# Optimization experiments

Hardware: AMD Instinct MI355X
Metric: run time of the kernel (lower is better)

Reference implementation:

```python
import jax, jax.numpy as jnp
import numpy as np

N_NODES = 50000
N_EDGES = 800000
D = 128
BN_EPS = 1e-5


def gcn_conv(x, src, dst, W, b, n_nodes):
    # x: [N, Din]; src/dst: [E+N] (self-loops already appended)
    h = x @ W  # [N, Dout]
    deg = jax.ops.segment_sum(jnp.ones_like(src, dtype=h.dtype), dst, num_segments=n_nodes)
    dinv = jnp.where(deg > 0, jax.lax.rsqrt(deg), 0.0)  # deg^{-1/2}
    norm = dinv[src] * dinv[dst]  # [E+N]
    msg = h[src] * norm[:, None]  # gather + scale
    out = jax.ops.segment_sum(msg, dst, num_segments=n_nodes)  # scatter-add
    return out + b


def batchnorm_prelu(x, gamma, beta, a):
    # training-mode BN over node dim (biased variance), then PReLU
    mu = jnp.mean(x, axis=0)
    var = jnp.mean(jnp.square(x - mu), axis=0)
    xn = (x - mu) * jax.lax.rsqrt(var + BN_EPS)
    y = xn * gamma + beta
    return jnp.where(y >= 0, y, a * y)


def setup_inputs():
    key = jax.random.key(0)
    ks = jax.random.split(key, 8)
    x = jax.random.normal(ks[0], (N_NODES, D), dtype=jnp.float32)
    edge_index = jax.random.randint(ks[1], (2, N_EDGES), 0, N_NODES, dtype=jnp.int32)
    lim = float(np.sqrt(6.0 / (D + D)))  # glorot
    W1 = jax.random.uniform(ks[2], (D, D), jnp.float32, -lim, lim)
    W2 = jax.random.uniform(ks[3], (D, D), jnp.float32, -lim, lim)
    b1 = jnp.zeros((D,), jnp.float32)
    b2 = jnp.zeros((D,), jnp.float32)
    gamma1 = jnp.ones((D,), jnp.float32)
    beta1 = jnp.zeros((D,), jnp.float32)
    gamma2 = jnp.ones((D,), jnp.float32)
    beta2 = jnp.zeros((D,), jnp.float32)
    a1 = jnp.full((1,), 0.25, jnp.float32)
    a2 = jnp.full((1,), 0.25, jnp.float32)
    return {"x": x, "edge_index": edge_index, "W1": W1, "b1": b1, "gamma1": gamma1,
            "beta1": beta1, "a1": a1, "W2": W2, "b2": b2, "gamma2": gamma2,
            "beta2": beta2, "a2": a2}


def reference(x, edge_index, W1, b1, gamma1, beta1, a1, W2, b2, gamma2, beta2, a2):
    n = x.shape[0]
    loops = jnp.arange(n, dtype=edge_index.dtype)
    src = jnp.concatenate([edge_index[0], loops])
    dst = jnp.concatenate([edge_index[1], loops])
    h = gcn_conv(x, src, dst, W1, b1, n)
    h = batchnorm_prelu(h, gamma1, beta1, a1)
    h = gcn_conv(h, src, dst, W2, b2, n)
    h = batchnorm_prelu(h, gamma2, beta2, a2)
    return h
```

## Files before the change

### kernel.cpp

```cpp
#include <hip/hip_runtime.h>
#include <hip/hip_bf16.h>

#define N_NODES 50000
#define N_EDGES 800000
#define D 128
#define BN_EPS 1e-5f
#define GEMM_ROWS 128
#define LDS_PITCH 136

#define BSH 8
#define NB 196
#define TILE 4096
#define NTILES ((N_EDGES + TILE - 1) / TILE)
#define REC_CAP 6144

typedef unsigned short u16;
typedef short bf16x8 __attribute__((ext_vector_type(8)));
typedef float f32x4  __attribute__((ext_vector_type(4)));

__device__ __forceinline__ u16 f2bf(float f) {
    union { float f; unsigned int u; } v; v.f = f;
    unsigned int u = v.u;
    return (u16)((u + 0x7FFF + ((u >> 16) & 1)) >> 16);
}
__device__ __forceinline__ float bflo(unsigned int u) {
    union { unsigned int u; float f; } v; v.u = u << 16; return v.f;
}
__device__ __forceinline__ float bfhi(unsigned int u) {
    union { unsigned int u; float f; } v; v.u = u & 0xFFFF0000u; return v.f;
}
__device__ __forceinline__ unsigned int packbf(float a, float b) {
    return (unsigned int)f2bf(a) | ((unsigned int)f2bf(b) << 16);
}

__global__ __launch_bounds__(256) void hist_prep(const int* __restrict__ dst,
                                                 const float* __restrict__ W1,
                                                 const float* __restrict__ W2,
                                                 int* __restrict__ thist,
                                                 u16* __restrict__ Wt1,
                                                 u16* __restrict__ Wt2,
                                                 float* __restrict__ sums) {
    __shared__ int h[256];
    const int t = threadIdx.x;
    const int b = blockIdx.x;
    if (b < NTILES) {
        h[t] = 0;
        __syncthreads();
        const int e0 = b * TILE;
#pragma unroll
        for (int i = 0; i < 16; ++i) {
            int e = e0 + t + 256 * i;
            if (e < N_EDGES) atomicAdd(&h[dst[e] >> BSH], 1);
        }
        __syncthreads();
        thist[b * 256 + t] = h[t];
    } else {
        const int wb = b - NTILES;
        if (wb == 0) { sums[t] = 0.f; sums[256 + t] = 0.f; }
        int u = wb * 256 + t;
        const float* W = (u < 16384) ? W1 : W2;
        u16* Wt        = (u < 16384) ? Wt1 : Wt2;
        int v = u & 16383;
        int k = v >> 7, n = v & 127;
        Wt[n * 128 + k] = f2bf(W[v]);
    }
}

__global__ __launch_bounds__(256) void bucket_scan(const int* __restrict__ thist,
                                                   int* __restrict__ btot,
                                                   int* __restrict__ bbase,
                                                   int* __restrict__ bcur,
                                                   int* __restrict__ row_ptr) {
    __shared__ int s[256];
    const int t = threadIdx.x;
    int v = 0;
    for (int i = 0; i < NTILES; ++i) v += thist[i * 256 + t];
    s[t] = v;
    __syncthreads();
#pragma unroll
    for (int off = 1; off < 256; off <<= 1) {
        int add = (t >= off) ? s[t - off] : 0;
        __syncthreads();
        s[t] += add;
        __syncthreads();
    }
    if (t < NB) { btot[t] = v; bbase[t] = s[t] - v; bcur[t] = s[t] - v; }
    if (t == 0) row_ptr[N_NODES] = N_EDGES;
}

__global__ __launch_bounds__(256) void bucket_scatter(const int* __restrict__ src,
                                                      const int* __restrict__ dst,
                                                      int* __restrict__ bcur,
                                                      unsigned int* __restrict__ brec) {
    __shared__ int h[256];
    __shared__ int sb[256];
    __shared__ int lbase[256];
    __shared__ int lcur[256];
    __shared__ int gbase[256];
    __shared__ unsigned int  rec[TILE];
    __shared__ unsigned char rbk[TILE];
    const int t  = threadIdx.x;
    const int e0 = blockIdx.x * TILE;
    const int tcount = min(TILE, N_EDGES - e0);

    h[t] = 0;
    __syncthreads();

    unsigned int myrec[16];
    int          myb[16];
#pragma unroll
    for (int i = 0; i < 16; ++i) {
        int e = e0 + t + 256 * i;
        if (e < N_EDGES) {
            unsigned int s_ = (unsigned int)src[e];
            unsigned int d_ = (unsigned int)dst[e];
            int b = (int)(d_ >> BSH);
            myb[i]   = b;
            myrec[i] = s_ | ((d_ & 255u) << 16);
            atomicAdd(&h[b], 1);
        } else myb[i] = -1;
    }
    __syncthreads();
    sb[t] = h[t];
    __syncthreads();
#pragma unroll
    for (int off = 1; off < 256; off <<= 1) {
        int add = (t >= off) ? sb[t - off] : 0;
        __syncthreads();
        sb[t] += add;
        __syncthreads();
    }
    lbase[t] = sb[t] - h[t];
    lcur[t]  = sb[t] - h[t];
    __syncthreads();
#pragma unroll
    for (int i = 0; i < 16; ++i) {
        if (myb[i] >= 0) {
            int p = atomicAdd(&lcur[myb[i]], 1);
            rec[p] = myrec[i];
            rbk[p] = (unsigned char)myb[i];
        }
    }
    __syncthreads();
    if (t < NB && h[t] > 0) gbase[t] = atomicAdd(&bcur[t], h[t]);
    __syncthreads();
    for (int i = t; i < tcount; i += 256) {
        int b = rbk[i];
        brec[gbase[b] + (i - lbase[b])] = rec[i];
    }
}

__global__ __launch_bounds__(256) void bucket_csr(const unsigned int* __restrict__ brec,
                                                  const int* __restrict__ bbase,
                                                  const int* __restrict__ btot,
                                                  int* __restrict__ row_ptr,
                                                  u16* __restrict__ col,
                                                  float* __restrict__ dinv) {
    __shared__ unsigned int rec[REC_CAP];
    __shared__ u16 cls[REC_CAP];
    __shared__ int h[256];
    __shared__ int sb[256];
    __shared__ int lcur[256];
    const int b    = blockIdx.x;
    const int t    = threadIdx.x;
    const int base = bbase[b];
    const int cnt  = min(btot[b], REC_CAP);
    const int n0   = b << BSH;
    const int nn   = min(256, N_NODES - n0);

    for (int i = t; i < cnt; i += 256) rec[i] = brec[base + i];
    h[t] = 0;
    __syncthreads();
    for (int i = t; i < cnt; i += 256) atomicAdd(&h[(rec[i] >> 16) & 255u], 1);
    __syncthreads();
    sb[t] = h[t];
    __syncthreads();
#pragma unroll
    for (int off = 1; off < 256; off <<= 1) {
        int add = (t >= off) ? sb[t - off] : 0;
        __syncthreads();
        sb[t] += add;
        __syncthreads();
    }
    int excl = sb[t] - h[t];
    lcur[t] = excl;
    if (t < nn) {
        row_ptr[n0 + t] = base + excl;
        dinv[n0 + t]    = rsqrtf((float)h[t] + 1.0f);
    }
    __syncthreads();
    for (int i = t; i < cnt; i += 256) {
        unsigned int r = rec[i];
        int p = atomicAdd(&lcur[(r >> 16) & 255u], 1);
        cls[p] = (u16)(r & 0xFFFFu);
    }
    __syncthreads();
    for (int i = t; i < cnt; i += 256) col[base + i] = cls[i];
}

template <bool BN_IN>
__global__ __launch_bounds__(256) void gemm_bf16(const void* __restrict__ Xv,
                                                 const u16* __restrict__ Wt,
                                                 u16* __restrict__ C,
                                                 const float* __restrict__ dinv,
                                                 const float* __restrict__ sums,
                                                 const float* __restrict__ gamma,
                                                 const float* __restrict__ beta,
                                                 const float* __restrict__ a,
                                                 int nrows) {
    __shared__ u16 As[GEMM_ROWS * LDS_PITCH];
    __shared__ u16 Ws[128 * LDS_PITCH];
    const int tid  = threadIdx.x;
    const int row0 = blockIdx.x * GEMM_ROWS;
    const float invN = 1.0f / (float)N_NODES;

    const bf16x8* Wt8 = (const bf16x8*)Wt;
#pragma unroll
    for (int i = 0; i < 8; ++i) {
        int u = tid + 256 * i;
        int n = u >> 4, kg = u & 15;
        *(bf16x8*)&Ws[n * LDS_PITCH + kg * 8] = Wt8[u];
    }

    if (BN_IN) {
        const uint4* X4 = (const uint4*)Xv;
        const float av = a[0];
#pragma unroll
        for (int i = 0; i < 8; ++i) {
            int u    = tid + 256 * i;
            int r    = u >> 4, kg = u & 15;
            int grow = row0 + r;
            uint4 o = make_uint4(0, 0, 0, 0);
            if (grow < nrows) {
                uint4 v = X4[(size_t)grow * 16 + kg];
                float f[8] = { bflo(v.x), bfhi(v.x), bflo(v.y), bfhi(v.y),
                               bflo(v.z), bfhi(v.z), bflo(v.w), bfhi(v.w) };
#pragma unroll
                for (int c = 0; c < 8; ++c) {
                    int fe     = kg * 8 + c;
                    float mean = sums[fe] * invN;
                    float var  = sums[128 + fe] * invN - mean * mean;
                    float sc   = rsqrtf(var + BN_EPS) * gamma[fe];
                    float y    = (f[c] - mean) * sc + beta[fe];
                    f[c]       = (y >= 0.f) ? y : av * y;
                }
                o.x = packbf(f[0], f[1]); o.y = packbf(f[2], f[3]);
                o.z = packbf(f[4], f[5]); o.w = packbf(f[6], f[7]);
            }
            *(uint4*)&As[r * LDS_PITCH + kg * 8] = o;
        }
    } else {
        const float4* X4 = (const float4*)Xv;
#pragma unroll
        for (int i = 0; i < 16; ++i) {
            int u    = tid + 256 * i;
            int r    = u >> 5, kf = u & 31;
            int grow = row0 + r;
            float4 v = make_float4(0.f, 0.f, 0.f, 0.f);
            if (grow < nrows) v = X4[(size_t)grow * 32 + kf];
            ushort4 p;
            p.x = f2bf(v.x); p.y = f2bf(v.y); p.z = f2bf(v.z); p.w = f2bf(v.w);
            *(ushort4*)&As[r * LDS_PITCH + kf * 4] = p;
        }
    }
    __syncthreads();

    const int wv   = tid >> 6;
    const int lane = tid & 63;
    const int n    = lane & 15;
    const int q    = lane >> 4;
    const int c0   = wv * 32;

    bf16x8 bfr[4][2];
#pragma unroll
    for (int kb = 0; kb < 4; ++kb)
#pragma unroll
        for (int c = 0; c < 2; ++c)
            bfr[kb][c] = *(const bf16x8*)&Ws[(c0 + 16 * c + n) * LDS_PITCH + 32 * kb + 8 * q];

    f32x4 acc[8][2];
    const f32x4 z = {0.f, 0.f, 0.f, 0.f};
#pragma unroll
    for (int rt = 0; rt < 8; ++rt) { acc[rt][0] = z; acc[rt][1] = z; }

#pragma unroll
    for (int kb = 0; kb < 4; ++kb) {
#pragma unroll
        for (int rt = 0; rt < 8; ++rt) {
            bf16x8 af = *(const bf16x8*)&As[(16 * rt + n) * LDS_PITCH + 32 * kb + 8 * q];
            acc[rt][0] = __builtin_amdgcn_mfma_f32_16x16x32_bf16(af, bfr[kb][0], acc[rt][0], 0, 0, 0);
            acc[rt][1] = __builtin_amdgcn_mfma_f32_16x16x32_bf16(af, bfr[kb][1], acc[rt][1], 0, 0, 0);
        }
    }

#pragma unroll
    for (int rt = 0; rt < 8; ++rt) {
        int gr0 = row0 + 16 * rt + 4 * q;
#pragma unroll
        for (int r = 0; r < 4; ++r) {
            int gr = gr0 + r;
            if (gr < nrows) {
                float dv = dinv[gr];
                C[(size_t)gr * D + c0 + n]      = f2bf(acc[rt][0][r] * dv);
                C[(size_t)gr * D + c0 + 16 + n] = f2bf(acc[rt][1][r] * dv);
            }
        }
    }
}

__global__ __launch_bounds__(256) void pull_agg(const u16* __restrict__ H,
                                                const int* __restrict__ row_ptr,
                                                const u16* __restrict__ col,
                                                const float* __restrict__ dinv,
                                                u16* __restrict__ out) {
    const int sub  = threadIdx.x & 15;
    const int grp  = (blockIdx.x * blockDim.x + threadIdx.x) >> 4;
    const int ngrp = (gridDim.x * blockDim.x) >> 4;
    const uint4* H4   = (const uint4*)H;
    uint4*       out4 = (uint4*)out;

    for (int d = grp; d < N_NODES; d += ngrp) {
        const int beg = row_ptr[d];
        const int end = row_ptr[d + 1];
        float a0[8], a1[8] = {}, a2[8] = {}, a3[8] = {};
        {
            uint4 v = H4[(size_t)d * 16 + sub];
            a0[0] = bflo(v.x); a0[1] = bfhi(v.x); a0[2] = bflo(v.y); a0[3] = bfhi(v.y);
            a0[4] = bflo(v.z); a0[5] = bfhi(v.z); a0[6] = bflo(v.w); a0[7] = bfhi(v.w);
        }
        int j = beg;
        for (; j + 3 < end; j += 4) {
            const int s0 = col[j], s1 = col[j + 1], s2 = col[j + 2], s3 = col[j + 3];
            const uint4 v0 = H4[(size_t)s0 * 16 + sub];
            const uint4 v1 = H4[(size_t)s1 * 16 + sub];
            const uint4 v2 = H4[(size_t)s2 * 16 + sub];
            const uint4 v3 = H4[(size_t)s3 * 16 + sub];
            a0[0] += bflo(v0.x); a0[1] += bfhi(v0.x); a0[2] += bflo(v0.y); a0[3] += bfhi(v0.y);
            a0[4] += bflo(v0.z); a0[5] += bfhi(v0.z); a0[6] += bflo(v0.w); a0[7] += bfhi(v0.w);
            a1[0] += bflo(v1.x); a1[1] += bfhi(v1.x); a1[2] += bflo(v1.y); a1[3] += bfhi(v1.y);
            a1[4] += bflo(v1.z); a1[5] += bfhi(v1.z); a1[6] += bflo(v1.w); a1[7] += bfhi(v1.w);
            a2[0] += bflo(v2.x); a2[1] += bfhi(v2.x); a2[2] += bflo(v2.y); a2[3] += bfhi(v2.y);
            a2[4] += bflo(v2.z); a2[5] += bfhi(v2.z); a2[6] += bflo(v2.w); a2[7] += bfhi(v2.w);
            a3[0] += bflo(v3.x); a3[1] += bfhi(v3.x); a3[2] += bflo(v3.y); a3[3] += bfhi(v3.y);
            a3[4] += bflo(v3.z); a3[5] += bfhi(v3.z); a3[6] += bflo(v3.w); a3[7] += bfhi(v3.w);
        }
        for (; j < end; ++j) {
            const uint4 v = H4[(size_t)col[j] * 16 + sub];
            a0[0] += bflo(v.x); a0[1] += bfhi(v.x); a0[2] += bflo(v.y); a0[3] += bfhi(v.y);
            a0[4] += bflo(v.z); a0[5] += bfhi(v.z); a0[6] += bflo(v.w); a0[7] += bfhi(v.w);
        }
        const float dv = dinv[d];
        float r[8];
#pragma unroll
        for (int c = 0; c < 8; ++c) r[c] = ((a0[c] + a1[c]) + (a2[c] + a3[c])) * dv;
        uint4 o;
        o.x = packbf(r[0], r[1]); o.y = packbf(r[2], r[3]);
        o.z = packbf(r[4], r[5]); o.w = packbf(r[6], r[7]);
        out4[(size_t)d * 16 + sub] = o;
    }
}

__global__ __launch_bounds__(256) void bn_reduce_bf(const u16* __restrict__ X,
                                                    float* __restrict__ sums, int n) {
    __shared__ float red[256];
    const int fp  = threadIdx.x & 63;
    const int rof = threadIdx.x >> 6;
    const unsigned int* X2 = (const unsigned int*)X;
    float s0 = 0.f, q0 = 0.f, s1 = 0.f, q1 = 0.f;
    for (int r = blockIdx.x * 4 + rof; r < n; r += gridDim.x * 4) {
        unsigned int u = X2[(size_t)r * 64 + fp];
        float v0 = bflo(u), v1 = bfhi(u);
        s0 += v0; q0 += v0 * v0; s1 += v1; q1 += v1 * v1;
    }
    red[threadIdx.x] = s0; __syncthreads();
    if (rof == 0) s0 = red[fp] + red[fp + 64] + red[fp + 128] + red[fp + 192];
    __syncthreads(); red[threadIdx.x] = q0; __syncthreads();
    if (rof == 0) q0 = red[fp] + red[fp + 64] + red[fp + 128] + red[fp + 192];
    __syncthreads(); red[threadIdx.x] = s1; __syncthreads();
    if (rof == 0) s1 = red[fp] + red[fp + 64] + red[fp + 128] + red[fp + 192];
    __syncthreads(); red[threadIdx.x] = q1; __syncthreads();
    if (rof == 0) {
        q1 = red[fp] + red[fp + 64] + red[fp + 128] + red[fp + 192];
        int f = fp * 2;
        atomicAdd(&sums[f], s0);       atomicAdd(&sums[128 + f], q0);
        atomicAdd(&sums[f + 1], s1);   atomicAdd(&sums[128 + f + 1], q1);
    }
}

__global__ void bn_prelu_bf(const u16* __restrict__ X, const float* __restrict__ sums,
                            const float* __restrict__ gamma, const float* __restrict__ beta,
                            const float* __restrict__ a, float* __restrict__ out,
                            float invN) {
    int idx = blockIdx.x * blockDim.x + threadIdx.x;
    if (idx >= N_NODES * 64) return;
    unsigned int u = ((const unsigned int*)X)[idx];
    int f0 = (idx * 2) & 127;
    float av = a[0];
    float2 o;
    {
        float mean = sums[f0] * invN;
        float var  = sums[128 + f0] * invN - mean * mean;
        float sc   = rsqrtf(var + BN_EPS) * gamma[f0];
        float y    = (bflo(u) - mean) * sc + beta[f0];
        o.x = (y >= 0.f) ? y : av * y;
    }
    {
        int f1 = f0 + 1;
        float mean = sums[f1] * invN;
        float var  = sums[128 + f1] * invN - mean * mean;
        float sc   = rsqrtf(var + BN_EPS) * gamma[f1];
        float y    = (bfhi(u) - mean) * sc + beta[f1];
        o.y = (y >= 0.f) ? y : av * y;
    }
    ((float2*)out)[idx] = o;
}

extern "C" void kernel_launch(void* const* d_in, const int* in_sizes, int n_in,
                              void* d_out, int out_size, void* d_ws, size_t ws_size,
                              hipStream_t stream) {
    const float* x      = (const float*)d_in[0];
    const int*   edges  = (const int*)d_in[1];
    const float* W1     = (const float*)d_in[2];
    const float* gamma1 = (const float*)d_in[4];
    const float* beta1  = (const float*)d_in[5];
    const float* a1     = (const float*)d_in[6];
    const float* W2     = (const float*)d_in[7];
    const float* gamma2 = (const float*)d_in[9];
    const float* beta2  = (const float*)d_in[10];
    const float* a2     = (const float*)d_in[11];

    const int* src = edges;
    const int* dst = edges + N_EDGES;

    float* OUT = (float*)d_out;
    char* ws = (char*)d_ws;
    u16*   Abf      = (u16*)ws;    ws += (size_t)N_NODES * D * sizeof(u16);
    u16*   Obf      = (u16*)ws;    ws += (size_t)N_NODES * D * sizeof(u16);
    float* dinv     = (float*)ws;  ws += N_NODES * sizeof(float);
    float* sums     = (float*)ws;  ws += 512 * sizeof(float);
    int*   row_ptr  = (int*)ws;    ws += (N_NODES + 1) * sizeof(int);
    int*   btot     = (int*)ws;    ws += NB * sizeof(int);
    int*   bbase    = (int*)ws;    ws += NB * sizeof(int);
    int*   bcur     = (int*)ws;    ws += NB * sizeof(int);
    int*   thist    = (int*)ws;    ws += (size_t)NTILES * 256 * sizeof(int);
    unsigned int* brec = (unsigned int*)ws; ws += (size_t)N_EDGES * sizeof(unsigned int);
    u16*   col      = (u16*)ws;    ws += (size_t)N_EDGES * sizeof(u16);
    u16*   Wt1      = (u16*)ws;    ws += 16384 * sizeof(u16);
    u16*   Wt2      = (u16*)ws;    ws += 16384 * sizeof(u16);

    const float invN = 1.0f / (float)N_NODES;
    const int gemmGrid = (N_NODES + GEMM_ROWS - 1) / GEMM_ROWS;
    const int prGrid   = (N_NODES * 64 + 255) / 256;

    hist_prep<<<NTILES + 128, 256, 0, stream>>>(dst, W1, W2, thist, Wt1, Wt2, sums);
    bucket_scan<<<1, 256, 0, stream>>>(thist, btot, bbase, bcur, row_ptr);
    bucket_scatter<<<NTILES, 256, 0, stream>>>(src, dst, bcur, brec);
    bucket_csr<<<NB, 256, 0, stream>>>(brec, bbase, btot, row_ptr, col, dinv);

    gemm_bf16<false><<<gemmGrid, 256, 0, stream>>>(x, Wt1, Abf, dinv,
                                                   nullptr, nullptr, nullptr, nullptr, N_NODES);
    pull_agg<<<2048, 256, 0, stream>>>(Abf, row_ptr, col, dinv, Obf);
    bn_reduce_bf<<<512, 256, 0, stream>>>(Obf, sums, N_NODES);

    gemm_bf16<true><<<gemmGrid, 256, 0, stream>>>(Obf, Wt2, Abf, dinv,
                                                  sums, gamma1, beta1, a1, N_NODES);
    pull_agg<<<2048, 256, 0, stream>>>(Abf, row_ptr, col, dinv, Obf);
    bn_reduce_bf<<<512, 256, 0, stream>>>(Obf, sums + 256, N_NODES);
    bn_prelu_bf<<<prGrid, 256, 0, stream>>>(Obf, sums + 256, gamma2, beta2, a2, OUT, invN);
}
```

Measured before the change: 304.2 us.

## Fuse all GCN stages into one cooperative persistent kernel with grid syncs

Replaces the eleven separate kernel launches with a single cooperative persistent kernel that runs every stage and separates them with grid.sync(). The first GEMM now runs alongside CSR construction, on the blocks not used for buckets. The dinv scaling moves into a separate elementwise pass after the GEMM, and the W tile is read straight from global memory instead of being staged in LDS. This removes launch gaps and tail effects but adds grid-wide barriers, caps occupancy at four blocks per CU, and adds an extra read-modify-write pass over the activations.

```diff
diff --git a/kernel.cpp b/kernel.cpp
--- a/kernel.cpp
+++ b/kernel.cpp
@@ -1,4 +1,5 @@
 #include <hip/hip_runtime.h>
+#include <hip/hip_cooperative_groups.h>
 #include <hip/hip_bf16.h>
 
 #define N_NODES 50000
@@ -7,6 +8,7 @@
 #define BN_EPS 1e-5f
 #define GEMM_ROWS 128
 #define LDS_PITCH 136
+#define NGT ((N_NODES + GEMM_ROWS - 1) / GEMM_ROWS)
 
 #define BSH 8
 #define NB 196
@@ -14,6 +16,8 @@
 #define NTILES ((N_EDGES + TILE - 1) / TILE)
 #define REC_CAP 6144
 
+#define SMEM_BYTES 39936
+
 typedef unsigned short u16;
 typedef short bf16x8 __attribute__((ext_vector_type(8)));
 typedef float f32x4  __attribute__((ext_vector_type(4)));
@@ -33,196 +37,30 @@
     return (unsigned int)f2bf(a) | ((unsigned int)f2bf(b) << 16);
 }
 
-__global__ __launch_bounds__(256) void hist_prep(const int* __restrict__ dst,
-                                                 const float* __restrict__ W1,
-                                                 const float* __restrict__ W2,
-                                                 int* __restrict__ thist,
-                                                 u16* __restrict__ Wt1,
-                                                 u16* __restrict__ Wt2,
-                                                 float* __restrict__ sums) {
-    __shared__ int h[256];
-    const int t = threadIdx.x;
-    const int b = blockIdx.x;
-    if (b < NTILES) {
-        h[t] = 0;
-        __syncthreads();
-        const int e0 = b * TILE;
-#pragma unroll
-        for (int i = 0; i < 16; ++i) {
-            int e = e0 + t + 256 * i;
-            if (e < N_EDGES) atomicAdd(&h[dst[e] >> BSH], 1);
-        }
-        __syncthreads();
-        thist[b * 256 + t] = h[t];
-    } else {
-        const int wb = b - NTILES;
-        if (wb == 0) { sums[t] = 0.f; sums[256 + t] = 0.f; }
-        int u = wb * 256 + t;
-        const float* W = (u < 16384) ? W1 : W2;
-        u16* Wt        = (u < 16384) ? Wt1 : Wt2;
-        int v = u & 16383;
-        int k = v >> 7, n = v & 127;
-        Wt[n * 128 + k] = f2bf(W[v]);
-    }
-}
-
-__global__ __launch_bounds__(256) void bucket_scan(const int* __restrict__ thist,
-                                                   int* __restrict__ btot,
-                                                   int* __restrict__ bbase,
-                                                   int* __restrict__ bcur,
-                                                   int* __restrict__ row_ptr) {
-    __shared__ int s[256];
-    const int t = threadIdx.x;
-    int v = 0;
-    for (int i = 0; i < NTILES; ++i) v += thist[i * 256 + t];
-    s[t] = v;
-    __syncthreads();
-#pragma unroll
-    for (int off = 1; off < 256; off <<= 1) {
-        int add = (t >= off) ? s[t - off] : 0;
-        __syncthreads();
-        s[t] += add;
-        __syncthreads();
-    }
-    if (t < NB) { btot[t] = v; bbase[t] = s[t] - v; bcur[t] = s[t] - v; }
-    if (t == 0) row_ptr[N_NODES] = N_EDGES;
-}
-
-__global__ __launch_bounds__(256) void bucket_scatter(const int* __restrict__ src,
-                                                      const int* __restrict__ dst,
-                                                      int* __restrict__ bcur,
-                                                      unsigned int* __restrict__ brec) {
-    __shared__ int h[256];
-    __shared__ int sb[256];
-    __shared__ int lbase[256];
-    __shared__ int lcur[256];
-    __shared__ int gbase[256];
-    __shared__ unsigned int  rec[TILE];
-    __shared__ unsigned char rbk[TILE];
-    const int t  = threadIdx.x;
-    const int e0 = blockIdx.x * TILE;
-    const int tcount = min(TILE, N_EDGES - e0);
-
-    h[t] = 0;
-    __syncthreads();
-
-    unsigned int myrec[16];
-    int          myb[16];
-#pragma unroll
-    for (int i = 0; i < 16; ++i) {
-        int e = e0 + t + 256 * i;
-        if (e < N_EDGES) {
-            unsigned int s_ = (unsigned int)src[e];
-            unsigned int d_ = (unsigned int)dst[e];
-            int b = (int)(d_ >> BSH);
-            myb[i]   = b;
-            myrec[i] = s_ | ((d_ & 255u) << 16);
-            atomicAdd(&h[b], 1);
-        } else myb[i] = -1;
-    }
-    __syncthreads();
-    sb[t] = h[t];
-    __syncthreads();
-#pragma unroll
-    for (int off = 1; off < 256; off <<= 1) {
-        int add = (t >= off) ? sb[t - off] : 0;
-        __syncthreads();
-        sb[t] += add;
-        __syncthreads();
-    }
-    lbase[t] = sb[t] - h[t];
-    lcur[t]  = sb[t] - h[t];
-    __syncthreads();
-#pragma unroll
-    for (int i = 0; i < 16; ++i) {
-        if (myb[i] >= 0) {
-            int p = atomicAdd(&lcur[myb[i]], 1);
-            rec[p] = myrec[i];
-            rbk[p] = (unsigned char)myb[i];
-        }
-    }
-    __syncthreads();
-    if (t < NB && h[t] > 0) gbase[t] = atomicAdd(&bcur[t], h[t]);
-    __syncthreads();
-    for (int i = t; i < tcount; i += 256) {
-        int b = rbk[i];
-        brec[gbase[b] + (i - lbase[b])] = rec[i];
-    }
-}
-
-__global__ __launch_bounds__(256) void bucket_csr(const unsigned int* __restrict__ brec,
-                                                  const int* __restrict__ bbase,
-                                                  const int* __restrict__ btot,
-                                                  int* __restrict__ row_ptr,
-                                                  u16* __restrict__ col,
-                                                  float* __restrict__ dinv) {
-    __shared__ unsigned int rec[REC_CAP];
-    __shared__ u16 cls[REC_CAP];
-    __shared__ int h[256];
-    __shared__ int sb[256];
-    __shared__ int lcur[256];
-    const int b    = blockIdx.x;
-    const int t    = threadIdx.x;
-    const int base = bbase[b];
-    const int cnt  = min(btot[b], REC_CAP);
-    const int n0   = b << BSH;
-    const int nn   = min(256, N_NODES - n0);
-
-    for (int i = t; i < cnt; i += 256) rec[i] = brec[base + i];
-    h[t] = 0;
-    __syncthreads();
-    for (int i = t; i < cnt; i += 256) atomicAdd(&h[(rec[i] >> 16) & 255u], 1);
-    __syncthreads();
-    sb[t] = h[t];
-    __syncthreads();
-#pragma unroll
-    for (int off = 1; off < 256; off <<= 1) {
-        int add = (t >= off) ? sb[t - off] : 0;
-        __syncthreads();
-        sb[t] += add;
-        __syncthreads();
-    }
-    int excl = sb[t] - h[t];
-    lcur[t] = excl;
-    if (t < nn) {
-        row_ptr[n0 + t] = base + excl;
-        dinv[n0 + t]    = rsqrtf((float)h[t] + 1.0f);
-    }
-    __syncthreads();
-    for (int i = t; i < cnt; i += 256) {
-        unsigned int r = rec[i];
-        int p = atomicAdd(&lcur[(r >> 16) & 255u], 1);
-        cls[p] = (u16)(r & 0xFFFFu);
-    }
-    __syncthreads();
-    for (int i = t; i < cnt; i += 256) col[base + i] = cls[i];
-}
-
-template <bool BN_IN>
-__global__ __launch_bounds__(256) void gemm_bf16(const void* __restrict__ Xv,
-                                                 const u16* __restrict__ Wt,
-                                                 u16* __restrict__ C,
-                                                 const float* __restrict__ dinv,
-                                                 const float* __restrict__ sums,
-                                                 const float* __restrict__ gamma,
-                                                 const float* __restrict__ beta,
-                                                 const float* __restrict__ a,
-                                                 int nrows) {
-    __shared__ u16 As[GEMM_ROWS * LDS_PITCH];
-    __shared__ u16 Ws[128 * LDS_PITCH];
+struct GcnP {
+    const float* x; const int* src; const int* dst;
+    const float* W1; const float* gamma1; const float* beta1; const float* a1;
+    const float* W2; const float* gamma2; const float* beta2; const float* a2;
+    float* OUT;
+    u16* Abf; u16* Obf; float* dinv; float* sums;
+    int* row_ptr; int* btot; int* bbase; int* bcur; int* thist;
+    unsigned int* brec; u16* col; u16* Wt1; u16* Wt2;
+};
+
+__device__ __forceinline__ void gemm_phase(char* smemc, int tile, const void* Xv,
+                                           const u16* __restrict__ Wt,
+                                           u16* __restrict__ C,
+                                           const float* __restrict__ dinv,
+                                           const float* __restrict__ sums,
+                                           const float* __restrict__ gamma,
+                                           const float* __restrict__ beta,
+                                           const float* __restrict__ a, bool bnin) {
+    u16* As = (u16*)smemc;
     const int tid  = threadIdx.x;
-    const int row0 = blockIdx.x * GEMM_ROWS;
+    const int row0 = tile * GEMM_ROWS;
     const float invN = 1.0f / (float)N_NODES;
 
-    const bf16x8* Wt8 = (const bf16x8*)Wt;
-#pragma unroll
-    for (int i = 0; i < 8; ++i) {
-        int u = tid + 256 * i;
-        int n = u >> 4, kg = u & 15;
-        *(bf16x8*)&Ws[n * LDS_PITCH + kg * 8] = Wt8[u];
-    }
-
-    if (BN_IN) {
+    if (bnin) {
         const uint4* X4 = (const uint4*)Xv;
         const float av = a[0];
 #pragma unroll
@@ -231,7 +69,7 @@
             int r    = u >> 4, kg = u & 15;
             int grow = row0 + r;
             uint4 o = make_uint4(0, 0, 0, 0);
-            if (grow < nrows) {
+            if (grow < N_NODES) {
                 uint4 v = X4[(size_t)grow * 16 + kg];
                 float f[8] = { bflo(v.x), bfhi(v.x), bflo(v.y), bfhi(v.y),
                                bflo(v.z), bfhi(v.z), bflo(v.w), bfhi(v.w) };
@@ -257,7 +95,7 @@
             int r    = u >> 5, kf = u & 31;
             int grow = row0 + r;
             float4 v = make_float4(0.f, 0.f, 0.f, 0.f);
-            if (grow < nrows) v = X4[(size_t)grow * 32 + kf];
+            if (grow < N_NODES) v = X4[(size_t)grow * 32 + kf];
             ushort4 p;
             p.x = f2bf(v.x); p.y = f2bf(v.y); p.z = f2bf(v.z); p.w = f2bf(v.w);
             *(ushort4*)&As[r * LDS_PITCH + kf * 4] = p;
@@ -276,7 +114,7 @@
     for (int kb = 0; kb < 4; ++kb)
 #pragma unroll
         for (int c = 0; c < 2; ++c)
-            bfr[kb][c] = *(const bf16x8*)&Ws[(c0 + 16 * c + n) * LDS_PITCH + 32 * kb + 8 * q];
+            bfr[kb][c] = *(const bf16x8*)&Wt[(size_t)(c0 + 16 * c + n) * 128 + 32 * kb + 8 * q];
 
     f32x4 acc[8][2];
     const f32x4 z = {0.f, 0.f, 0.f, 0.f};
@@ -299,23 +137,24 @@
 #pragma unroll
         for (int r = 0; r < 4; ++r) {
             int gr = gr0 + r;
-            if (gr < nrows) {
-                float dv = dinv[gr];
+            if (gr < N_NODES) {
+                float dv = dinv ? dinv[gr] : 1.0f;
                 C[(size_t)gr * D + c0 + n]      = f2bf(acc[rt][0][r] * dv);
                 C[(size_t)gr * D + c0 + 16 + n] = f2bf(acc[rt][1][r] * dv);
             }
         }
     }
-}
-
-__global__ __launch_bounds__(256) void pull_agg(const u16* __restrict__ H,
-                                                const int* __restrict__ row_ptr,
-                                                const u16* __restrict__ col,
-                                                const float* __restrict__ dinv,
-                                                u16* __restrict__ out) {
+    __syncthreads();
+}
+
+__device__ __forceinline__ void pull_phase(const u16* __restrict__ H,
+                                           const int* __restrict__ row_ptr,
+                                           const u16* __restrict__ col,
+                                           const float* __restrict__ dinv,
+                                           u16* __restrict__ out, int GD) {
     const int sub  = threadIdx.x & 15;
-    const int grp  = (blockIdx.x * blockDim.x + threadIdx.x) >> 4;
-    const int ngrp = (gridDim.x * blockDim.x) >> 4;
+    const int grp  = ((int)blockIdx.x * 256 + (int)threadIdx.x) >> 4;
+    const int ngrp = GD * 16;
     const uint4* H4   = (const uint4*)H;
     uint4*       out4 = (uint4*)out;
 
@@ -360,14 +199,14 @@
     }
 }
 
-__global__ __launch_bounds__(256) void bn_reduce_bf(const u16* __restrict__ X,
-                                                    float* __restrict__ sums, int n) {
-    __shared__ float red[256];
+__device__ __forceinline__ void bnred_phase(char* smemc, const u16* __restrict__ X,
+                                            float* __restrict__ sums, int GD) {
+    float* red = (float*)smemc;
     const int fp  = threadIdx.x & 63;
     const int rof = threadIdx.x >> 6;
     const unsigned int* X2 = (const unsigned int*)X;
     float s0 = 0.f, q0 = 0.f, s1 = 0.f, q1 = 0.f;
-    for (int r = blockIdx.x * 4 + rof; r < n; r += gridDim.x * 4) {
+    for (int r = (int)blockIdx.x * 4 + rof; r < N_NODES; r += GD * 4) {
         unsigned int u = X2[(size_t)r * 64 + fp];
         float v0 = bflo(u), v1 = bfhi(u);
         s0 += v0; q0 += v0 * v0; s1 += v1; q1 += v1 * v1;
@@ -385,86 +224,271 @@
         atomicAdd(&sums[f], s0);       atomicAdd(&sums[128 + f], q0);
         atomicAdd(&sums[f + 1], s1);   atomicAdd(&sums[128 + f + 1], q1);
     }
-}
-
-__global__ void bn_prelu_bf(const u16* __restrict__ X, const float* __restrict__ sums,
-                            const float* __restrict__ gamma, const float* __restrict__ beta,
-                            const float* __restrict__ a, float* __restrict__ out,
-                            float invN) {
-    int idx = blockIdx.x * blockDim.x + threadIdx.x;
-    if (idx >= N_NODES * 64) return;
-    unsigned int u = ((const unsigned int*)X)[idx];
-    int f0 = (idx * 2) & 127;
-    float av = a[0];
-    float2 o;
+    __syncthreads();
+}
+
+__global__ __launch_bounds__(256, 4) void gcn_mega(GcnP P) {
+    namespace cg = cooperative_groups;
+    cg::grid_group grid = cg::this_grid();
+    __shared__ __align__(16) char smem[SMEM_BYTES];
+    const int b  = blockIdx.x;
+    const int t  = threadIdx.x;
+    const int GD = (int)gridDim.x;
+    const float invN = 1.0f / (float)N_NODES;
+
+    if (b < NTILES) {
+        int* h = (int*)smem;
+        h[t] = 0;
+        __syncthreads();
+        const int e0 = b * TILE;
+#pragma unroll
+        for (int i = 0; i < 16; ++i) {
+            int e = e0 + t + 256 * i;
+            if (e < N_EDGES) atomicAdd(&h[P.dst[e] >> BSH], 1);
+        }
+        __syncthreads();
+        P.thist[b * 256 + t] = h[t];
+    } else if (b < NTILES + 128) {
+        int u = (b - NTILES) * 256 + t;
+        const float* W = (u < 16384) ? P.W1 : P.W2;
+        u16* Wt        = (u < 16384) ? P.Wt1 : P.Wt2;
+        int v = u & 16383;
+        int k = v >> 7, n = v & 127;
+        Wt[n * 128 + k] = f2bf(W[v]);
+    } else if (b == NTILES + 128) {
+        P.sums[t] = 0.f; P.sums[256 + t] = 0.f;
+    }
+    grid.sync();
+
+    if (b < NB) {
+        int* sh = (int*)smem;
+        sh[t] = (t < NTILES) ? P.thist[t * 256 + b] : 0;
+        __syncthreads();
+        for (int off = 128; off > 0; off >>= 1) {
+            if (t < off) sh[t] += sh[t + off];
+            __syncthreads();
+        }
+        if (t == 0) P.btot[b] = sh[0];
+    }
+    grid.sync();
+
+    if (b == 0) {
+        int* s = (int*)smem;
+        int v = (t < NB) ? P.btot[t] : 0;
+        s[t] = v;
+        __syncthreads();
+        for (int off = 1; off < 256; off <<= 1) {
+            int add = (t >= off) ? s[t - off] : 0;
+            __syncthreads();
+            s[t] += add;
+            __syncthreads();
+        }
+        if (t < NB) { P.bbase[t] = s[t] - v; P.bcur[t] = s[t] - v; }
+        if (t == 0) P.row_ptr[N_NODES] = N_EDGES;
+    }
+    grid.sync();
+
+    if (b < NTILES) {
+        unsigned int*  rec   = (unsigned int*)smem;
+        unsigned char* rbk   = (unsigned char*)(smem + 16384);
+        int* h     = (int*)(smem + 20480);
+        int* sb    = (int*)(smem + 21504);
+        int* lbase = (int*)(smem + 22528);
+        int* lcur  = (int*)(smem + 23552);
+        int* gbase = (int*)(smem + 24576);
+        const int e0 = b * TILE;
+        const int tcount = min(TILE, N_EDGES - e0);
+
+        h[t] = 0;
+        __syncthreads();
+        unsigned int myrec[16];
+        int          myb[16];
+#pragma unroll
+        for (int i = 0; i < 16; ++i) {
+            int e = e0 + t + 256 * i;
+            if (e < N_EDGES) {
+                unsigned int s_ = (unsigned int)P.src[e];
+                unsigned int d_ = (unsigned int)P.dst[e];
+                int bb = (int)(d_ >> BSH);
+                myb[i]   = bb;
+                myrec[i] = s_ | ((d_ & 255u) << 16);
+                atomicAdd(&h[bb], 1);
+            } else myb[i] = -1;
+        }
+        __syncthreads();
+        sb[t] = h[t];
+        __syncthreads();
+        for (int off = 1; off < 256; off <<= 1) {
+            int add = (t >= off) ? sb[t - off] : 0;
+            __syncthreads();
+            sb[t] += add;
+            __syncthreads();
+        }
+        lbase[t] = sb[t] - h[t];
+        lcur[t]  = sb[t] - h[t];
+        __syncthreads();
+#pragma unroll
+        for (int i = 0; i < 16; ++i) {
+            if (myb[i] >= 0) {
+                int p = atomicAdd(&lcur[myb[i]], 1);
+                rec[p] = myrec[i];
+                rbk[p] = (unsigned char)myb[i];
+            }
+        }
+        __syncthreads();
+        if (t < NB && h[t] > 0) gbase[t] = atomicAdd(&P.bcur[t], h[t]);
+        __syncthreads();
+        for (int i = t; i < tcount; i += 256) {
+            int bb = rbk[i];
+            P.brec[gbase[bb] + (i - lbase[bb])] = rec[i];
+        }
+        __syncthreads();
+    }
+    grid.sync();
+
+    if (b < NB) {
+        unsigned int* rec = (unsigned int*)smem;
+        u16* cls   = (u16*)(smem + 24576);
+        int* h     = (int*)(smem + 36864);
+        int* sb    = (int*)(smem + 37888);
+        int* lcur  = (int*)(smem + 38912);
+        const int base = P.bbase[b];
+        const int cnt  = min(P.btot[b], REC_CAP);
+        const int n0   = b << BSH;
+        const int nn   = min(256, N_NODES - n0);
+
+        for (int i = t; i < cnt; i += 256) rec[i] = P.brec[base + i];
+        h[t] = 0;
+        __syncthreads();
+        for (int i = t; i < cnt; i += 256) atomicAdd(&h[(rec[i] >> 16) & 255u], 1);
+        __syncthreads();
+        sb[t] = h[t];
+        __syncthreads();
+        for (int off = 1; off < 256; off <<= 1) {
+            int add = (t >= off) ? sb[t - off] : 0;
+            __syncthreads();
+            sb[t] += add;
+            __syncthreads();
+        }
+        int excl = sb[t] - h[t];
+        lcur[t] = excl;
+        if (t < nn) {
+            P.row_ptr[n0 + t] = base + excl;
+            P.dinv[n0 + t]    = rsqrtf((float)h[t] + 1.0f);
+        }
+        __syncthreads();
+        for (int i = t; i < cnt; i += 256) {
+            unsigned int r = rec[i];
+            int p = atomicAdd(&lcur[(r >> 16) & 255u], 1);
+            cls[p] = (u16)(r & 0xFFFFu);
+        }
+        __syncthreads();
+        for (int i = t; i < cnt; i += 256) P.col[base + i] = cls[i];
+        __syncthreads();
+    } else {
+        for (int tile = b - NB; tile < NGT; tile += GD - NB)
+            gemm_phase(smem, tile, P.x, P.Wt1, P.Abf, nullptr,
+                       nullptr, nullptr, nullptr, nullptr, false);
+    }
+    grid.sync();
+
     {
-        float mean = sums[f0] * invN;
-        float var  = sums[128 + f0] * invN - mean * mean;
-        float sc   = rsqrtf(var + BN_EPS) * gamma[f0];
-        float y    = (bflo(u) - mean) * sc + beta[f0];
-        o.x = (y >= 0.f) ? y : av * y;
-    }
+        unsigned int* A2 = (unsigned int*)P.Abf;
+        for (int idx = b * 256 + t; idx < N_NODES * 64; idx += GD * 256) {
+            int row = idx >> 6;
+            float dv = P.dinv[row];
+            unsigned int u = A2[idx];
+            A2[idx] = packbf(bflo(u) * dv, bfhi(u) * dv);
+        }
+    }
+    grid.sync();
+
+    pull_phase(P.Abf, P.row_ptr, P.col, P.dinv, P.Obf, GD);
+    grid.sync();
+
+    bnred_phase(smem, P.Obf, P.sums, GD);
+    grid.sync();
+
+    for (int tile = b; tile < NGT; tile += GD)
+        gemm_phase(smem, tile, P.Obf, P.Wt2, P.Abf, P.dinv,
+                   P.sums, P.gamma1, P.beta1, P.a1, true);
+    grid.sync();
+
+    pull_phase(P.Abf, P.row_ptr, P.col, P.dinv, P.Obf, GD);
+    grid.sync();
+
+    bnred_phase(smem, P.Obf, P.sums + 256, GD);
+    grid.sync();
+
     {
-        int f1 = f0 + 1;
-        float mean = sums[f1] * invN;
-        float var  = sums[128 + f1] * invN - mean * mean;
-        float sc   = rsqrtf(var + BN_EPS) * gamma[f1];
-        float y    = (bfhi(u) - mean) * sc + beta[f1];
-        o.y = (y >= 0.f) ? y : av * y;
-    }
-    ((float2*)out)[idx] = o;
+        const unsigned int* X2 = (const unsigned int*)P.Obf;
+        const float* sums = P.sums + 256;
+        const float av = P.a2[0];
+        float2* O2 = (float2*)P.OUT;
+        for (int idx = b * 256 + t; idx < N_NODES * 64; idx += GD * 256) {
+            unsigned int u = X2[idx];
+            int f0 = (idx * 2) & 127;
+            int f1 = f0 + 1;
+            float2 o;
+            {
+                float mean = sums[f0] * invN;
+                float var  = sums[128 + f0] * invN - mean * mean;
+                float sc   = rsqrtf(var + BN_EPS) * P.gamma2[f0];
+                float y    = (bflo(u) - mean) * sc + P.beta2[f0];
+                o.x = (y >= 0.f) ? y : av * y;
+            }
+            {
+                float mean = sums[f1] * invN;
+                float var  = sums[128 + f1] * invN - mean * mean;
+                float sc   = rsqrtf(var + BN_EPS) * P.gamma2[f1];
+                float y    = (bfhi(u) - mean) * sc + P.beta2[f1];
+                o.y = (y >= 0.f) ? y : av * y;
+            }
+            O2[idx] = o;
+        }
+    }
 }
 
 extern "C" void kernel_launch(void* const* d_in, const int* in_sizes, int n_in,
                               void* d_out, int out_size, void* d_ws, size_t ws_size,
                               hipStream_t stream) {
-    const float* x      = (const float*)d_in[0];
-    const int*   edges  = (const int*)d_in[1];
-    const float* W1     = (const float*)d_in[2];
-    const float* gamma1 = (const float*)d_in[4];
-    const float* beta1  = (const float*)d_in[5];
-    const float* a1     = (const float*)d_in[6];
-    const float* W2     = (const float*)d_in[7];
-    const float* gamma2 = (const float*)d_in[9];
-    const float* beta2  = (const float*)d_in[10];
-    const float* a2     = (const float*)d_in[11];
-
-    const int* src = edges;
-    const int* dst = edges + N_EDGES;
-
-    float* OUT = (float*)d_out;
+    GcnP P;
+    P.x      = (const float*)d_in[0];
+    const int* edges = (const int*)d_in[1];
+    P.W1     = (const float*)d_in[2];
+    P.gamma1 = (const float*)d_in[4];
+    P.beta1  = (const float*)d_in[5];
+    P.a1     = (const float*)d_in[6];
+    P.W2     = (const float*)d_in[7];
+    P.gamma2 = (const float*)d_in[9];
+    P.beta2  = (const float*)d_in[10];
+    P.a2     = (const float*)d_in[11];
+    P.src = edges;
+    P.dst = edges + N_EDGES;
+    P.OUT = (float*)d_out;
+
     char* ws = (char*)d_ws;
-    u16*   Abf      = (u16*)ws;    ws += (size_t)N_NODES * D * sizeof(u16);
-    u16*   Obf      = (u16*)ws;    ws += (size_t)N_NODES * D * sizeof(u16);
-    float* dinv     = (float*)ws;  ws += N_NODES * sizeof(float);
-    float* sums     = (float*)ws;  ws += 512 * sizeof(float);
-    int*   row_ptr  = (int*)ws;    ws += (N_NODES + 1) * sizeof(int);
-    int*   btot     = (int*)ws;    ws += NB * sizeof(int);
-    int*   bbase    = (int*)ws;    ws += NB * sizeof(int);
-    int*   bcur     = (int*)ws;    ws += NB * sizeof(int);
-    int*   thist    = (int*)ws;    ws += (size_t)NTILES * 256 * sizeof(int);
-    unsigned int* brec = (unsigned int*)ws; ws += (size_t)N_EDGES * sizeof(unsigned int);
-    u16*   col      = (u16*)ws;    ws += (size_t)N_EDGES * sizeof(u16);
-    u16*   Wt1      = (u16*)ws;    ws += 16384 * sizeof(u16);
-    u16*   Wt2      = (u16*)ws;    ws += 16384 * sizeof(u16);
-
-    const float invN = 1.0f / (float)N_NODES;
-    const int gemmGrid = (N_NODES + GEMM_ROWS - 1) / GEMM_ROWS;
-    const int prGrid   = (N_NODES * 64 + 255) / 256;
-
-    hist_prep<<<NTILES + 128, 256, 0, stream>>>(dst, W1, W2, thist, Wt1, Wt2, sums);
-    bucket_scan<<<1, 256, 0, stream>>>(thist, btot, bbase, bcur, row_ptr);
-    bucket_scatter<<<NTILES, 256, 0, stream>>>(src, dst, bcur, brec);
-    bucket_csr<<<NB, 256, 0, stream>>>(brec, bbase, btot, row_ptr, col, dinv);
-
-    gemm_bf16<false><<<gemmGrid, 256, 0, stream>>>(x, Wt1, Abf, dinv,
-                                                   nullptr, nullptr, nullptr, nullptr, N_NODES);
-    pull_agg<<<2048, 256, 0, stream>>>(Abf, row_ptr, col, dinv, Obf);
-    bn_reduce_bf<<<512, 256, 0, stream>>>(Obf, sums, N_NODES);
-
-    gemm_bf16<true><<<gemmGrid, 256, 0, stream>>>(Obf, Wt2, Abf, dinv,
-                                                  sums, gamma1, beta1, a1, N_NODES);
-    pull_agg<<<2048, 256, 0, stream>>>(Abf, row_ptr, col, dinv, Obf);
-    bn_reduce_bf<<<512, 256, 0, stream>>>(Obf, sums + 256, N_NODES);
-    bn_prelu_bf<<<prGrid, 256, 0, stream>>>(Obf, sums + 256, gamma2, beta2, a2, OUT, invN);
-}
+    P.Abf     = (u16*)ws;    ws += (size_t)N_NODES * D * sizeof(u16);
+    P.Obf     = (u16*)ws;    ws += (size_t)N_NODES * D * sizeof(u16);
+    P.dinv    = (float*)ws;  ws += N_NODES * sizeof(float);
+    P.sums    = (float*)ws;  ws += 512 * sizeof(float);
+    P.row_ptr = (int*)ws;    ws += (N_NODES + 1) * sizeof(int);
+    P.btot    = (int*)ws;    ws += 256 * sizeof(int);
+    P.bbase   = (int*)ws;    ws += 256 * sizeof(int);
+    P.bcur    = (int*)ws;    ws += 256 * sizeof(int);
+    P.thist   = (int*)ws;    ws += (size_t)NTILES * 256 * sizeof(int);
+    P.brec    = (unsigned int*)ws; ws += (size_t)N_EDGES * sizeof(unsigned int);
+    P.col     = (u16*)ws;    ws += (size_t)N_EDGES * sizeof(u16);
+    P.Wt1     = (u16*)ws;    ws += 16384 * sizeof(u16);
+    P.Wt2     = (u16*)ws;    ws += 16384 * sizeof(u16);
+
+    int nb = 0;
+    (void)hipOccupancyMaxActiveBlocksPerMultiprocessor(&nb, (const void*)gcn_mega, 256, 0);
+    int grid = 1024;
+    if (nb > 0 && nb * 256 < grid) grid = nb * 256;
+    if (grid < NTILES + 129 + 1) grid = NTILES + 130;
+
+    void* args[] = { &P };
+    (void)hipLaunchCooperativeKernel((const void*)gcn_mega, dim3(grid), dim3(256),
+                                     args, 0, stream);
+}
```

After: 948.4 us. 212% more time.

## Co-schedule edge bucket scatter with first GEMM and fold dinv scaling into CSR build

Applied to the files above, without the earlier changes.

Merges the bucket scatter and the first X·W1 GEMM into a single launch whose blocks split by index, so the independent graph-preprocessing and GEMM work can run concurrently on the GPU. Because the GEMM no longer waits for dinv, the dinv row scaling moves into the CSR-build kernel, which rescales each Abf row by rsqrt(deg+1) right after computing the degrees. This removes one launch and lets the GEMM overlap the scatter. The cost is an extra read-modify-write pass over Abf, one more bf16 rounding step, and a large static LDS allocation for every block of the merged kernel, including the scatter blocks that use much less.

```diff
diff --git a/kernel.cpp b/kernel.cpp
--- a/kernel.cpp
+++ b/kernel.cpp
@@ -7,6 +7,7 @@
 #define BN_EPS 1e-5f
 #define GEMM_ROWS 128
 #define LDS_PITCH 136
+#define NGT ((N_NODES + GEMM_ROWS - 1) / GEMM_ROWS)
 
 #define BSH 8
 #define NB 196
@@ -88,130 +89,19 @@
     if (t == 0) row_ptr[N_NODES] = N_EDGES;
 }
 
-__global__ __launch_bounds__(256) void bucket_scatter(const int* __restrict__ src,
-                                                      const int* __restrict__ dst,
-                                                      int* __restrict__ bcur,
-                                                      unsigned int* __restrict__ brec) {
-    __shared__ int h[256];
-    __shared__ int sb[256];
-    __shared__ int lbase[256];
-    __shared__ int lcur[256];
-    __shared__ int gbase[256];
-    __shared__ unsigned int  rec[TILE];
-    __shared__ unsigned char rbk[TILE];
-    const int t  = threadIdx.x;
-    const int e0 = blockIdx.x * TILE;
-    const int tcount = min(TILE, N_EDGES - e0);
-
-    h[t] = 0;
-    __syncthreads();
-
-    unsigned int myrec[16];
-    int          myb[16];
-#pragma unroll
-    for (int i = 0; i < 16; ++i) {
-        int e = e0 + t + 256 * i;
-        if (e < N_EDGES) {
-            unsigned int s_ = (unsigned int)src[e];
-            unsigned int d_ = (unsigned int)dst[e];
-            int b = (int)(d_ >> BSH);
-            myb[i]   = b;
-            myrec[i] = s_ | ((d_ & 255u) << 16);
-            atomicAdd(&h[b], 1);
-        } else myb[i] = -1;
-    }
-    __syncthreads();
-    sb[t] = h[t];
-    __syncthreads();
-#pragma unroll
-    for (int off = 1; off < 256; off <<= 1) {
-        int add = (t >= off) ? sb[t - off] : 0;
-        __syncthreads();
-        sb[t] += add;
-        __syncthreads();
-    }
-    lbase[t] = sb[t] - h[t];
-    lcur[t]  = sb[t] - h[t];
-    __syncthreads();
-#pragma unroll
-    for (int i = 0; i < 16; ++i) {
-        if (myb[i] >= 0) {
-            int p = atomicAdd(&lcur[myb[i]], 1);
-            rec[p] = myrec[i];
-            rbk[p] = (unsigned char)myb[i];
-        }
-    }
-    __syncthreads();
-    if (t < NB && h[t] > 0) gbase[t] = atomicAdd(&bcur[t], h[t]);
-    __syncthreads();
-    for (int i = t; i < tcount; i += 256) {
-        int b = rbk[i];
-        brec[gbase[b] + (i - lbase[b])] = rec[i];
-    }
-}
-
-__global__ __launch_bounds__(256) void bucket_csr(const unsigned int* __restrict__ brec,
-                                                  const int* __restrict__ bbase,
-                                                  const int* __restrict__ btot,
-                                                  int* __restrict__ row_ptr,
-                                                  u16* __restrict__ col,
-                                                  float* __restrict__ dinv) {
-    __shared__ unsigned int rec[REC_CAP];
-    __shared__ u16 cls[REC_CAP];
-    __shared__ int h[256];
-    __shared__ int sb[256];
-    __shared__ int lcur[256];
-    const int b    = blockIdx.x;
-    const int t    = threadIdx.x;
-    const int base = bbase[b];
-    const int cnt  = min(btot[b], REC_CAP);
-    const int n0   = b << BSH;
-    const int nn   = min(256, N_NODES - n0);
-
-    for (int i = t; i < cnt; i += 256) rec[i] = brec[base + i];
-    h[t] = 0;
-    __syncthreads();
-    for (int i = t; i < cnt; i += 256) atomicAdd(&h[(rec[i] >> 16) & 255u], 1);
-    __syncthreads();
-    sb[t] = h[t];
-    __syncthreads();
-#pragma unroll
-    for (int off = 1; off < 256; off <<= 1) {
-        int add = (t >= off) ? sb[t - off] : 0;
-        __syncthreads();
-        sb[t] += add;
-        __syncthreads();
-    }
-    int excl = sb[t] - h[t];
-    lcur[t] = excl;
-    if (t < nn) {
-        row_ptr[n0 + t] = base + excl;
-        dinv[n0 + t]    = rsqrtf((float)h[t] + 1.0f);
-    }
-    __syncthreads();
-    for (int i = t; i < cnt; i += 256) {
-        unsigned int r = rec[i];
-        int p = atomicAdd(&lcur[(r >> 16) & 255u], 1);
-        cls[p] = (u16)(r & 0xFFFFu);
-    }
-    __syncthreads();
-    for (int i = t; i < cnt; i += 256) col[base + i] = cls[i];
-}
-
 template <bool BN_IN>
-__global__ __launch_bounds__(256) void gemm_bf16(const void* __restrict__ Xv,
-                                                 const u16* __restrict__ Wt,
-                                                 u16* __restrict__ C,
-                                                 const float* __restrict__ dinv,
-                                                 const float* __restrict__ sums,
-                                                 const float* __restrict__ gamma,
-                                                 const float* __restrict__ beta,
-                                                 const float* __restrict__ a,
-                                                 int nrows) {
-    __shared__ u16 As[GEMM_ROWS * LDS_PITCH];
-    __shared__ u16 Ws[128 * LDS_PITCH];
+__device__ __forceinline__ void gemm_tile(char* smemc, int tile, const void* Xv,
+                                          const u16* __restrict__ Wt,
+                                          u16* __restrict__ C,
+                                          const float* __restrict__ dinv,
+                                          const float* __restrict__ sums,
+                                          const float* __restrict__ gamma,
+                                          const float* __restrict__ beta,
+                                          const float* __restrict__ a) {
+    u16* As = (u16*)smemc;
+    u16* Ws = (u16*)(smemc + 34816);
     const int tid  = threadIdx.x;
-    const int row0 = blockIdx.x * GEMM_ROWS;
+    const int row0 = tile * GEMM_ROWS;
     const float invN = 1.0f / (float)N_NODES;
 
     const bf16x8* Wt8 = (const bf16x8*)Wt;
@@ -231,7 +121,7 @@
             int r    = u >> 4, kg = u & 15;
             int grow = row0 + r;
             uint4 o = make_uint4(0, 0, 0, 0);
-            if (grow < nrows) {
+            if (grow < N_NODES) {
                 uint4 v = X4[(size_t)grow * 16 + kg];
                 float f[8] = { bflo(v.x), bfhi(v.x), bflo(v.y), bfhi(v.y),
                                bflo(v.z), bfhi(v.z), bflo(v.w), bfhi(v.w) };
@@ -257,7 +147,7 @@
             int r    = u >> 5, kf = u & 31;
             int grow = row0 + r;
             float4 v = make_float4(0.f, 0.f, 0.f, 0.f);
-            if (grow < nrows) v = X4[(size_t)grow * 32 + kf];
+            if (grow < N_NODES) v = X4[(size_t)grow * 32 + kf];
             ushort4 p;
             p.x = f2bf(v.x); p.y = f2bf(v.y); p.z = f2bf(v.z); p.w = f2bf(v.w);
             *(ushort4*)&As[r * LDS_PITCH + kf * 4] = p;
@@ -299,13 +189,156 @@
 #pragma unroll
         for (int r = 0; r < 4; ++r) {
             int gr = gr0 + r;
-            if (gr < nrows) {
-                float dv = dinv[gr];
+            if (gr < N_NODES) {
+                float dv = dinv ? dinv[gr] : 1.0f;
                 C[(size_t)gr * D + c0 + n]      = f2bf(acc[rt][0][r] * dv);
                 C[(size_t)gr * D + c0 + 16 + n] = f2bf(acc[rt][1][r] * dv);
             }
         }
     }
+}
+
+__global__ __launch_bounds__(256) void scatter_gemm1(const int* __restrict__ src,
+                                                     const int* __restrict__ dst,
+                                                     int* __restrict__ bcur,
+                                                     unsigned int* __restrict__ brec,
+                                                     const float* __restrict__ x,
+                                                     const u16* __restrict__ Wt1,
+                                                     u16* __restrict__ Abf) {
+    __shared__ __align__(16) char smem[69632];
+    const int t = threadIdx.x;
+    const int b = blockIdx.x;
+
+    if (b >= NTILES) {
+        gemm_tile<false>(smem, b - NTILES, x, Wt1, Abf,
+                         nullptr, nullptr, nullptr, nullptr, nullptr);
+        return;
+    }
+
+    unsigned int*  rec   = (unsigned int*)smem;
+    unsigned char* rbk   = (unsigned char*)(smem + 16384);
+    int* h     = (int*)(smem + 20480);
+    int* sb    = (int*)(smem + 21504);
+    int* lbase = (int*)(smem + 22528);
+    int* lcur  = (int*)(smem + 23552);
+    int* gbase = (int*)(smem + 24576);
+    const int e0 = b * TILE;
+    const int tcount = min(TILE, N_EDGES - e0);
+
+    h[t] = 0;
+    __syncthreads();
+    unsigned int myrec[16];
+    int          myb[16];
+#pragma unroll
+    for (int i = 0; i < 16; ++i) {
+        int e = e0 + t + 256 * i;
+        if (e < N_EDGES) {
+            unsigned int s_ = (unsigned int)src[e];
+            unsigned int d_ = (unsigned int)dst[e];
+            int bb = (int)(d_ >> BSH);
+            myb[i]   = bb;
+            myrec[i] = s_ | ((d_ & 255u) << 16);
+            atomicAdd(&h[bb], 1);
+        } else myb[i] = -1;
+    }
+    __syncthreads();
+    sb[t] = h[t];
+    __syncthreads();
+#pragma unroll
+    for (int off = 1; off < 256; off <<= 1) {
+        int add = (t >= off) ? sb[t - off] : 0;
+        __syncthreads();
+        sb[t] += add;
+        __syncthreads();
+    }
+    lbase[t] = sb[t] - h[t];
+    lcur[t]  = sb[t] - h[t];
+    __syncthreads();
+#pragma unroll
+    for (int i = 0; i < 16; ++i) {
+        if (myb[i] >= 0) {
+            int p = atomicAdd(&lcur[myb[i]], 1);
+            rec[p] = myrec[i];
+            rbk[p] = (unsigned char)myb[i];
+        }
+    }
+    __syncthreads();
+    if (t < NB && h[t] > 0) gbase[t] = atomicAdd(&bcur[t], h[t]);
+    __syncthreads();
+    for (int i = t; i < tcount; i += 256) {
+        int bb = rbk[i];
+        brec[gbase[bb] + (i - lbase[bb])] = rec[i];
+    }
+}
+
+__global__ __launch_bounds__(256) void bucket_csr_scale(const unsigned int* __restrict__ brec,
+                                                        const int* __restrict__ bbase,
+                                                        const int* __restrict__ btot,
+                                                        int* __restrict__ row_ptr,
+                                                        u16* __restrict__ col,
+                                                        float* __restrict__ dinv,
+                                                        u16* __restrict__ Abf) {
+    __shared__ unsigned int rec[REC_CAP];
+    __shared__ u16 cls[REC_CAP];
+    __shared__ int h[256];
+    __shared__ int sb[256];
+    __shared__ int lcur[256];
+    const int b    = blockIdx.x;
+    const int t    = threadIdx.x;
+    const int base = bbase[b];
+    const int cnt  = min(btot[b], REC_CAP);
+    const int n0   = b << BSH;
+    const int nn   = min(256, N_NODES - n0);
+
+    for (int i = t; i < cnt; i += 256) rec[i] = brec[base + i];
+    h[t] = 0;
+    __syncthreads();
+    for (int i = t; i < cnt; i += 256) atomicAdd(&h[(rec[i] >> 16) & 255u], 1);
+    __syncthreads();
+    sb[t] = h[t];
+    __syncthreads();
+#pragma unroll
+    for (int off = 1; off < 256; off <<= 1) {
+        int add = (t >= off) ? sb[t - off] : 0;
+        __syncthreads();
+        sb[t] += add;
+        __syncthreads();
+    }
+    int excl = sb[t] - h[t];
+    lcur[t] = excl;
+    if (t < nn) {
+        row_ptr[n0 + t] = base + excl;
+        dinv[n0 + t]    = rsqrtf((float)h[t] + 1.0f);
+    }
+    __syncthreads();
+    for (int i = t; i < cnt; i += 256) {
+        unsigned int r = rec[i];
+        int p = atomicAdd(&lcur[(r >> 16) & 255u], 1);
+        cls[p] = (u16)(r & 0xFFFFu);
+    }
+    __syncthreads();
+    for (int i = t; i < cnt; i += 256) col[base + i] = cls[i];
+
+    unsigned int* A2 = (unsigned int*)Abf;
+    for (int i = t; i < nn * 64; i += 256) {
+        int r = i >> 6;
+        float dv = rsqrtf((float)h[r] + 1.0f);
+        size_t idx = (size_t)(n0 + r) * 64 + (i & 63);
+        unsigned int u = A2[idx];
+        A2[idx] = packbf(bflo(u) * dv, bfhi(u) * dv);
+    }
+}
+
+__global__ __launch_bounds__(256) void gemm2_k(const u16* __restrict__ Obf,
+                                               const u16* __restrict__ Wt2,
+                                               u16* __restrict__ Abf,
+                                               const float* __restrict__ dinv,
+                                               const float* __restrict__ sums,
+                                               const float* __restrict__ gamma1,
+                                               const float* __restrict__ beta1,
+                                               const float* __restrict__ a1) {
+    __shared__ __align__(16) char smem[69632];
+    gemm_tile<true>(smem, blockIdx.x, Obf, Wt2, Abf, dinv, sums, gamma1, beta1, a1);
 }
 
 __global__ __launch_bounds__(256) void pull_agg(const u16* __restrict__ H,
@@ -439,9 +472,9 @@
     float* dinv     = (float*)ws;  ws += N_NODES * sizeof(float);
     float* sums     = (float*)ws;  ws += 512 * sizeof(float);
     int*   row_ptr  = (int*)ws;    ws += (N_NODES + 1) * sizeof(int);
-    int*   btot     = (int*)ws;    ws += NB * sizeof(int);
-    int*   bbase    = (int*)ws;    ws += NB * sizeof(int);
-    int*   bcur     = (int*)ws;    ws += NB * sizeof(int);
+    int*   btot     = (int*)ws;    ws += 256 * sizeof(int);
+    int*   bbase    = (int*)ws;    ws += 256 * sizeof(int);
+    int*   bcur     = (int*)ws;    ws += 256 * sizeof(int);
     int*   thist    = (int*)ws;    ws += (size_t)NTILES * 256 * sizeof(int);
     unsigned int* brec = (unsigned int*)ws; ws += (size_t)N_EDGES * sizeof(unsigned int);
     u16*   col      = (u16*)ws;    ws += (size_t)N_EDGES * sizeof(u16);
@@ -449,21 +482,17 @@
     u16*   Wt2      = (u16*)ws;    ws += 16384 * sizeof(u16);
 
     const float invN = 1.0f / (float)N_NODES;
-    const int gemmGrid = (N_NODES + GEMM_ROWS - 1) / GEMM_ROWS;
-    const int prGrid   = (N_NODES * 64 + 255) / 256;
+    const int prGrid = (N_NODES * 64 + 255) / 256;
 
     hist_prep<<<NTILES + 128, 256, 0, stream>>>(dst, W1, W2, thist, Wt1, Wt2, sums);
     bucket_scan<<<1, 256, 0, stream>>>(thist, btot, bbase, bcur, row_ptr);
-    bucket_scatter<<<NTILES, 256, 0, stream>>>(src, dst, bcur, brec);
-    bucket_csr<<<NB, 256, 0, stream>>>(brec, bbase, btot, row_ptr, col, dinv);
-
-    gemm_bf16<false><<<gemmGrid, 256, 0, stream>>>(x, Wt1, Abf, dinv,
-                                                   nullptr, nullptr, nullptr, nullptr, N_NODES);
+    scatter_gemm1<<<NTILES + NGT, 256, 0, stream>>>(src, dst, bcur, brec, x, Wt1, Abf);
+    bucket_csr_scale<<<NB, 256, 0, stream>>>(brec, bbase, btot, row_ptr, col, dinv, Abf);
+
     pull_agg<<<2048, 256, 0, stream>>>(Abf, row_ptr, col, dinv, Obf);
     bn_reduce_bf<<<512, 256, 0, stream>>>(Obf, sums, N_NODES);
 
-    gemm_bf16<true><<<gemmGrid, 256, 0, stream>>>(Obf, Wt2, Abf, dinv,
-                                                  sums, gamma1, beta1, a1, N_NODES);
+    gemm2_k<<<NGT, 256, 0, stream>>>(Obf, Wt2, Abf, dinv, sums, gamma1, beta1, a1);
     pull_agg<<<2048, 256, 0, stream>>>(Abf, row_ptr, col, dinv, Obf);
     bn_reduce_bf<<<512, 256, 0, stream>>>(Obf, sums + 256, N_NODES);
     bn_prelu_bf<<<prGrid, 256, 0, stream>>>(Obf, sums + 256, gamma2, beta2, a2, OUT, invN);
```

Measured after the change: 313.2 us. 1.03x slower.
